# Kernel tuning notes

Measured on AMD Instinct MI355X. Metric: run time of the kernel, lower is better.

## Reference

```python
import jax, jax.numpy as jnp
import numpy as np

B, L, M, IS = 64, 20, 16, 1024  # batch, headers/example, tokens/header, feature dim
EPS = 1e-12


def setup_inputs() -> dict:
    key = jax.random.key(0)
    ks = jax.random.split(key, 10)
    total = B * L
    s = 1.0 / np.sqrt(IS)
    return {
        "ctx": jax.random.normal(ks[0], (B, IS), jnp.float32),
        "wemb_hpu": jax.random.normal(ks[1], (total, M, IS), jnp.float32),
        "l_hpu": jnp.full((total,), M, jnp.int32),
        "l_hs": jnp.full((B,), L, jnp.int32),
        "U_w": jax.random.uniform(ks[2], (IS, IS), jnp.float32, -s, s),
        "U_b": jnp.zeros((IS,), jnp.float32),
        "V_w": jax.random.uniform(ks[3], (IS, IS), jnp.float32, -s, s),
        "V_b": jnp.zeros((IS,), jnp.float32),
        "enc_w": jax.random.uniform(ks[4], (IS, 2 * IS), jnp.float32, -s, s),
        "enc_b": jnp.zeros((IS,), jnp.float32),
        "gamma": jnp.ones((IS,), jnp.float32),
        "beta": jnp.zeros((IS,), jnp.float32),
    }


def reference(ctx, wemb_hpu, l_hpu, l_hs, U_w, U_b, V_w, V_b, enc_w, enc_b, gamma, beta):
    total = wemb_hpu.shape[0]
    bS = ctx.shape[0]
    seg = jnp.repeat(jnp.arange(bS), total // bS)  # header-unit -> example id (constant l_hs)
    wenc_u = ctx @ U_w.T + U_b                      # [B, IS]
    wenc_v = wemb_hpu @ V_w.T + V_b                 # [T, M, IS]
    # per-header attention over its M tokens: sum over feature dim, softmax over tokens
    attn = jnp.einsum('ti,tmi->tm', wenc_u[seg], wenc_v)   # [T, M]
    p = jax.nn.softmax(attn, axis=1)
    pooled = jnp.einsum('tm,tmi->ti', p, wemb_hpu)          # [T, IS]
    cat = jnp.concatenate([pooled, ctx[seg]], axis=-1)      # [T, 2*IS]
    h = cat @ enc_w.T + enc_b                               # [T, IS]
    # scatter into padded [B, mL_hs, IS] (constant lengths -> exact reshape)
    wenc_hs = h.reshape(bS, total // bS, -1)
    # TF-style LayerNorm (eps inside sqrt)
    u = wenc_hs.mean(-1, keepdims=True)
    s2 = ((wenc_hs - u) ** 2).mean(-1, keepdims=True)
    x = (wenc_hs - u) / jnp.sqrt(s2 + EPS)
    return gamma * x + beta
```

## Files before the change

kernel.cpp:

```cpp
#include <hip/hip_runtime.h>
#include <math.h>

#define TPB 256

constexpr int ISZ = 1024;
constexpr int NB  = 64;
constexpr int NL  = 20;
constexpr int NM  = 16;
constexpr int NT  = NB * NL;

typedef __attribute__((ext_vector_type(8))) short  bf16x8;
typedef __attribute__((ext_vector_type(4))) float  f32x4;

__device__ __forceinline__ unsigned short f2bf(float x) {
    unsigned int u = __builtin_bit_cast(unsigned int, x);
    unsigned int r = (u + 0x7fff + ((u >> 16) & 1)) >> 16;
    return (unsigned short)r;
}
__device__ __forceinline__ float bf2f(unsigned short h) {
    unsigned int u = ((unsigned int)h) << 16;
    return __builtin_bit_cast(float, u);
}
__device__ __forceinline__ void split4(float4 v, ushort4& h, ushort4& l) {
    h.x = f2bf(v.x); l.x = f2bf(v.x - bf2f(h.x));
    h.y = f2bf(v.y); l.y = f2bf(v.y - bf2f(h.y));
    h.z = f2bf(v.z); l.z = f2bf(v.z - bf2f(h.z));
    h.w = f2bf(v.w); l.w = f2bf(v.w - bf2f(h.w));
}
__device__ __forceinline__ void gld_lds16(const void* g, void* l) {
    __builtin_amdgcn_global_load_lds(
        (const __attribute__((address_space(1))) unsigned int*)g,
        (__attribute__((address_space(3))) unsigned int*)l, 16, 0, 0);
}


__device__ __forceinline__ void stage_hl(const float* __restrict__ src, int ld,
                                         int kbeg, unsigned char* ldsH,
                                         unsigned char* ldsL, int tid)
{
    #pragma unroll
    for (int r = 0; r < 4; ++r) {
        int idx = r * 256 + tid;
        int row = idx >> 4, cg = (idx & 15) << 2;
        float4 v = *(const float4*)&src[(size_t)row * ld + kbeg + cg];
        ushort4 h, l; split4(v, h, l);
        int boff = row * 128 + ((cg << 1) ^ ((row & 7) << 4));
        *(ushort4*)(ldsH + boff) = h;
        *(ushort4*)(ldsL + boff) = l;
    }
}
__device__ __forceinline__ void stage_h(const float* __restrict__ src, int ld,
                                        int kbeg, unsigned char* ldsH, int tid)
{
    #pragma unroll
    for (int r = 0; r < 4; ++r) {
        int idx = r * 256 + tid;
        int row = idx >> 4, cg = (idx & 15) << 2;
        float4 v = *(const float4*)&src[(size_t)row * ld + kbeg + cg];
        ushort4 h = { f2bf(v.x), f2bf(v.y), f2bf(v.z), f2bf(v.w) };
        int boff = row * 128 + ((cg << 1) ^ ((row & 7) << 4));
        *(ushort4*)(ldsH + boff) = h;
    }
}

__device__ __forceinline__ void comp_hl(const unsigned char* lds, f32x4 acc[2][2], int tid)
{
    const int wid = tid >> 6, lane = tid & 63;
    const int ln = lane & 15, kb = lane >> 4;
    const int wr = wid >> 1, wc = wid & 1;
    #pragma unroll
    for (int ks = 0; ks < 2; ++ks) {
        const int cb = ks * 64 + kb * 16;
        bf16x8 ah[2], al[2], bh[2], bl[2];
        #pragma unroll
        for (int m = 0; m < 2; ++m) {
            int ra = wr * 32 + m * 16 + ln;
            int off = ra * 128 + (cb ^ ((ra & 7) << 4));
            ah[m] = *(const bf16x8*)(lds + off);
            al[m] = *(const bf16x8*)(lds + 8192 + off);
        }
        #pragma unroll
        for (int n = 0; n < 2; ++n) {
            int rb = wc * 32 + n * 16 + ln;
            int off = rb * 128 + (cb ^ ((rb & 7) << 4));
            bh[n] = *(const bf16x8*)(lds + 16384 + off);
            bl[n] = *(const bf16x8*)(lds + 24576 + off);
        }
        #pragma unroll
        for (int m = 0; m < 2; ++m)
            #pragma unroll
            for (int n = 0; n < 2; ++n) {
                acc[m][n] = __builtin_amdgcn_mfma_f32_16x16x32_bf16(ah[m], bh[n], acc[m][n], 0, 0, 0);
                acc[m][n] = __builtin_amdgcn_mfma_f32_16x16x32_bf16(ah[m], bl[n], acc[m][n], 0, 0, 0);
                acc[m][n] = __builtin_amdgcn_mfma_f32_16x16x32_bf16(al[m], bh[n], acc[m][n], 0, 0, 0);
            }
    }
}
__device__ __forceinline__ void comp_h(const unsigned char* lds, f32x4 acc[2][2], int tid)
{
    const int wid = tid >> 6, lane = tid & 63;
    const int ln = lane & 15, kb = lane >> 4;
    const int wr = wid >> 1, wc = wid & 1;
    #pragma unroll
    for (int ks = 0; ks < 2; ++ks) {
        const int cb = ks * 64 + kb * 16;
        bf16x8 ah[2], bh[2];
        #pragma unroll
        for (int m = 0; m < 2; ++m) {
            int ra = wr * 32 + m * 16 + ln;
            ah[m] = *(const bf16x8*)(lds + ra * 128 + (cb ^ ((ra & 7) << 4)));
        }
        #pragma unroll
        for (int n = 0; n < 2; ++n) {
            int rb = wc * 32 + n * 16 + ln;
            bh[n] = *(const bf16x8*)(lds + 16384 + rb * 128 + (cb ^ ((rb & 7) << 4)));
        }
        #pragma unroll
        for (int m = 0; m < 2; ++m)
            #pragma unroll
            for (int n = 0; n < 2; ++n)
                acc[m][n] = __builtin_amdgcn_mfma_f32_16x16x32_bf16(ah[m], bh[n], acc[m][n], 0, 0, 0);
    }
}

__global__ __launch_bounds__(TPB)
void init_small(float* __restrict__ wenc_u, float* __restrict__ cenc,
                float* __restrict__ uv,
                const float* __restrict__ U_b, const float* __restrict__ enc_b)
{
    int i = blockIdx.x * TPB + threadIdx.x;
    int i4 = i << 2;
    int col = i4 & (ISZ - 1);
    if (i4 < NB * ISZ) {
        *(float4*)&wenc_u[i4] = *(const float4*)&U_b[col];
    } else if (i4 < 2 * NB * ISZ) {
        *(float4*)&cenc[i4 - NB * ISZ] = *(const float4*)&enc_b[col];
    } else {
        float4 z = {0.f, 0.f, 0.f, 0.f};
        *(float4*)&uv[i4 - 2 * NB * ISZ] = z;
    }
}

__global__ __launch_bounds__(TPB)
void small_and_vt(const float* __restrict__ ctx, const float* __restrict__ U_w,
                  const float* __restrict__ enc_w, const float* __restrict__ V_w,
                  float* __restrict__ wenc_u, float* __restrict__ cenc,
                  unsigned short* __restrict__ Vth, unsigned short* __restrict__ Vtl)
{
    __shared__ __align__(16) unsigned char smem[32768];
    const int tid = threadIdx.x;
    const int bid = blockIdx.x;

    if (bid >= 256) {
        float (*t)[65] = (float(*)[65])smem;
        const int id = bid - 256;
        const int r0 = (id >> 4) * 64, c0 = (id & 15) * 64;
        const int tr = tid >> 4, tc = (tid & 15) * 4;
        #pragma unroll
        for (int i = 0; i < 4; ++i) {
            float4 v = *(const float4*)&V_w[(size_t)(r0 + tr + 16 * i) * ISZ + c0 + tc];
            t[tr + 16 * i][tc + 0] = v.x; t[tr + 16 * i][tc + 1] = v.y;
            t[tr + 16 * i][tc + 2] = v.z; t[tr + 16 * i][tc + 3] = v.w;
        }
        __syncthreads();
        #pragma unroll
        for (int i = 0; i < 4; ++i) {
            int rr = tr + 16 * i;
            float4 v = { t[tc + 0][rr], t[tc + 1][rr], t[tc + 2][rr], t[tc + 3][rr] };
            ushort4 h, l; split4(v, h, l);
            *(ushort4*)&Vth[(size_t)(c0 + rr) * ISZ + r0 + tc] = h;
            *(ushort4*)&Vtl[(size_t)(c0 + rr) * ISZ + r0 + tc] = l;
        }
        return;
    }

    const int n0 = (bid & 15) * 64;
    const int yv = bid >> 4;
    const bool isU = (yv >= 8);
    const int kbeg = (isU ? (yv - 8) : yv) * 128;

    f32x4 acc[2][2] = {};
    for (int kt = 0; kt < 2; ++kt) {
        const int kk = kbeg + kt * 64;
        if (isU) {
            stage_hl(ctx, ISZ, kk, smem, smem + 8192, tid);
            stage_hl(U_w + (size_t)n0 * ISZ, ISZ, kk, smem + 16384, smem + 24576, tid);
        } else {
            stage_h(ctx, ISZ, kk, smem, tid);
            stage_h(enc_w + (size_t)n0 * 2048 + 1024, 2048, kk, smem + 16384, tid);
        }
        __syncthreads();
        if (isU) comp_hl(smem, acc, tid);
        else     comp_h(smem, acc, tid);
        __syncthreads();
    }

    const int wid = tid >> 6, lane = tid & 63;
    const int wr = wid >> 1, wc = wid & 1;
    const int cl = lane & 15, rg = lane >> 4;
    float* dst = isU ? wenc_u : cenc;
    #pragma unroll
    for (int m = 0; m < 2; ++m)
        #pragma unroll
        for (int n = 0; n < 2; ++n) {
            int col = n0 + wc * 32 + n * 16 + cl;
            #pragma unroll
            for (int j = 0; j < 4; ++j) {
                int row = wr * 32 + m * 16 + rg * 4 + j;
                atomicAdd(&dst[(size_t)row * ISZ + col], acc[m][n][j]);
            }
        }
}

__global__ __launch_bounds__(TPB)
void gemm_uv(const float* __restrict__ wenc_u,
             const unsigned short* __restrict__ Vth,
             const unsigned short* __restrict__ Vtl,
             float* __restrict__ uv)
{
    __shared__ __align__(16) unsigned char smem[32768];
    const int tid = threadIdx.x;
    const int n0 = blockIdx.x * 64;
    const int kbeg = blockIdx.y * 128;
    const int wid = tid >> 6, lane = tid & 63;
    const int srow = lane >> 3, sbyte = (lane & 7) << 4;
    const int swz = sbyte ^ (srow << 4);

    f32x4 acc[2][2] = {};
    for (int kt = 0; kt < 2; ++kt) {
        const int kk = kbeg + kt * 64;
        const int kbyte = kk * 2;
        #pragma unroll
        for (int i = 0; i < 2; ++i) {
            int r = wid * 8 + i * 32 + srow;
            size_t gb = (size_t)(n0 + r) * 2048 + kbyte + swz;
            gld_lds16((const char*)Vth + gb, (void*)(smem + 16384 + wid * 1024 + i * 4096));
            gld_lds16((const char*)Vtl + gb, (void*)(smem + 24576 + wid * 1024 + i * 4096));
        }
        stage_hl(wenc_u, ISZ, kk, smem, smem + 8192, tid);
        __syncthreads();
        comp_hl(smem, acc, tid);
        __syncthreads();
    }

    const int wr = wid >> 1, wc = wid & 1;
    const int cl = lane & 15, rg = lane >> 4;
    #pragma unroll
    for (int m = 0; m < 2; ++m)
        #pragma unroll
        for (int n = 0; n < 2; ++n) {
            int col = n0 + wc * 32 + n * 16 + cl;
            #pragma unroll
            for (int j = 0; j < 4; ++j) {
                int row = wr * 32 + m * 16 + rg * 4 + j;
                atomicAdd(&uv[(size_t)row * ISZ + col], acc[m][n][j]);
            }
        }
}

__global__ __launch_bounds__(TPB)
void attn_encconv(const float* __restrict__ wemb, const float* __restrict__ uv,
                  unsigned short* __restrict__ pooledb,
                  const float* __restrict__ enc_w, unsigned short* __restrict__ encb)
{
    if (blockIdx.x >= NT) {
        const int row = blockIdx.x - NT;
        const int c = threadIdx.x << 2;
        float4 v = *(const float4*)&enc_w[(size_t)row * 2048 + c];
        ushort4 o = { f2bf(v.x), f2bf(v.y), f2bf(v.z), f2bf(v.w) };
        *(ushort4*)&encb[(size_t)row * ISZ + c] = o;
        return;
    }
    const int t   = blockIdx.x;
    const int b   = t / NL;
    const int tid = threadIdx.x;
    const int lane = tid & 63, wid = tid >> 6;
    __shared__ float red[16][4];
    __shared__ float att[16];

    const float* w = wemb + (size_t)t * NM * ISZ;
    const int j0 = tid << 2;
    float4 u4 = *(const float4*)&uv[(size_t)b * ISZ + j0];

    float4 wv[NM];
    float part[NM];
    #pragma unroll
    for (int m = 0; m < NM; ++m) {
        wv[m] = *(const float4*)&w[m * ISZ + j0];
        part[m] = wv[m].x * u4.x + wv[m].y * u4.y + wv[m].z * u4.z + wv[m].w * u4.w;
    }
    #pragma unroll
    for (int m = 0; m < NM; ++m) {
        float v = part[m];
        #pragma unroll
        for (int off = 32; off > 0; off >>= 1) v += __shfl_down(v, off, 64);
        if (lane == 0) red[m][wid] = v;
    }
    __syncthreads();
    if (tid < NM) att[tid] = red[tid][0] + red[tid][1] + red[tid][2] + red[tid][3];
    __syncthreads();

    float mx = att[0];
    #pragma unroll
    for (int m = 1; m < NM; ++m) mx = fmaxf(mx, att[m]);
    float p[NM], s = 0.0f;
    #pragma unroll
    for (int m = 0; m < NM; ++m) { p[m] = __expf(att[m] - mx); s += p[m]; }
    float inv = 1.0f / s;

    float4 acc = {0.0f, 0.0f, 0.0f, 0.0f};
    #pragma unroll
    for (int m = 0; m < NM; ++m) {
        float pm = p[m] * inv;
        acc.x += pm * wv[m].x; acc.y += pm * wv[m].y;
        acc.z += pm * wv[m].z; acc.w += pm * wv[m].w;
    }
    ushort4 o;
    o.x = f2bf(acc.x); o.y = f2bf(acc.y); o.z = f2bf(acc.z); o.w = f2bf(acc.w);
    *(ushort4*)&pooledb[(size_t)t * ISZ + j0] = o;
}

__global__ __launch_bounds__(TPB)
void gemm_enc_mfma(const unsigned short* __restrict__ Abf,
                   const unsigned short* __restrict__ Bbf,
                   const float* __restrict__ cenc,
                   float* __restrict__ C)
{
    __shared__ __align__(16) unsigned char lds[24576];
    const int tid  = threadIdx.x;
    const int wid  = tid >> 6, lane = tid & 63;
    const int m0   = blockIdx.y * 128;
    const int n0   = blockIdx.x * 64;
    const int ln   = lane & 15, kb = lane >> 4;
    const int wr   = wid >> 1, wc = wid & 1;
    const int srow = lane >> 3, sbyte = (lane & 7) << 4;
    const int swz  = sbyte ^ (srow << 4);

    f32x4 acc[4][2] = {};
    const char* Abase = (const char*)Abf;
    const char* Bbase = (const char*)Bbf;

    for (int kt = 0; kt < 16; ++kt) {
        const int kbyte = kt * 128;
        #pragma unroll
        for (int i = 0; i < 4; ++i) {
            int r = wid * 8 + i * 32 + srow;
            gld_lds16(Abase + ((size_t)(m0 + r) * ISZ) * 2 + kbyte + swz,
                      (void*)(lds + wid * 1024 + i * 4096));
        }
        #pragma unroll
        for (int i = 0; i < 2; ++i) {
            int r = wid * 8 + i * 32 + srow;
            gld_lds16(Bbase + ((size_t)(n0 + r) * ISZ) * 2 + kbyte + swz,
                      (void*)(lds + 16384 + wid * 1024 + i * 4096));
        }
        __syncthreads();

        #pragma unroll
        for (int ks = 0; ks < 2; ++ks) {
            const int cb = (ks * 64 + kb * 16);
            bf16x8 a[4], b[2];
            #pragma unroll
            for (int m = 0; m < 4; ++m) {
                int ra = wr * 64 + m * 16 + ln;
                a[m] = *(const bf16x8*)(lds + ra * 128 + (cb ^ ((ra & 7) << 4)));
            }
            #pragma unroll
            for (int n = 0; n < 2; ++n) {
                int rb = wc * 32 + n * 16 + ln;
                b[n] = *(const bf16x8*)(lds + 16384 + rb * 128 + (cb ^ ((rb & 7) << 4)));
            }
            #pragma unroll
            for (int m = 0; m < 4; ++m)
                #pragma unroll
                for (int n = 0; n < 2; ++n)
                    acc[m][n] = __builtin_amdgcn_mfma_f32_16x16x32_bf16(a[m], b[n], acc[m][n], 0, 0, 0);
        }
        __syncthreads();
    }

    const int cl = lane & 15, rg = lane >> 4;
    #pragma unroll
    for (int m = 0; m < 4; ++m) {
        #pragma unroll
        for (int n = 0; n < 2; ++n) {
            int col = n0 + wc * 32 + n * 16 + cl;
            #pragma unroll
            for (int j = 0; j < 4; ++j) {
                int row = m0 + wr * 64 + m * 16 + rg * 4 + j;
                C[(size_t)row * ISZ + col] = acc[m][n][j] + cenc[(size_t)(row / NL) * ISZ + col];
            }
        }
    }
}

__global__ __launch_bounds__(TPB)
void layernorm_inplace(float* __restrict__ x, const float* __restrict__ gamma,
                       const float* __restrict__ beta)
{
    __shared__ float rs[4], rs2[4];
    __shared__ float mu_s, rstd_s;
    const int t = blockIdx.x;
    const int tid = threadIdx.x;
    const int lane = tid & 63, wid = tid >> 6;
    const int c = tid << 2;

    float4 v = *(const float4*)&x[(size_t)t * ISZ + c];
    float s  = v.x + v.y + v.z + v.w;
    float s2 = v.x * v.x + v.y * v.y + v.z * v.z + v.w * v.w;
    #pragma unroll
    for (int off = 32; off > 0; off >>= 1) {
        s  += __shfl_down(s, off, 64);
        s2 += __shfl_down(s2, off, 64);
    }
    if (lane == 0) { rs[wid] = s; rs2[wid] = s2; }
    __syncthreads();
    if (tid == 0) {
        float S  = rs[0] + rs[1] + rs[2] + rs[3];
        float S2 = rs2[0] + rs2[1] + rs2[2] + rs2[3];
        float m  = S / ISZ;
        float var = S2 / ISZ - m * m;
        mu_s  = m;
        rstd_s = rsqrtf(var + 1e-12f);
    }
    __syncthreads();
    const float mu = mu_s, rstd = rstd_s;
    float4 g  = *(const float4*)&gamma[c];
    float4 be = *(const float4*)&beta[c];
    float4 o;
    o.x = g.x * (v.x - mu) * rstd + be.x;
    o.y = g.y * (v.y - mu) * rstd + be.y;
    o.z = g.z * (v.z - mu) * rstd + be.z;
    o.w = g.w * (v.w - mu) * rstd + be.w;
    *(float4*)&x[(size_t)t * ISZ + c] = o;
}

extern "C" void kernel_launch(void* const* d_in, const int* in_sizes, int n_in,
                              void* d_out, int out_size, void* d_ws, size_t ws_size,
                              hipStream_t stream)
{
    const float* ctx   = (const float*)d_in[0];
    const float* wemb  = (const float*)d_in[1];
    const float* U_w   = (const float*)d_in[4];
    const float* U_b   = (const float*)d_in[5];
    const float* V_w   = (const float*)d_in[6];
    const float* enc_w = (const float*)d_in[8];
    const float* enc_b = (const float*)d_in[9];
    const float* gamma = (const float*)d_in[10];
    const float* beta  = (const float*)d_in[11];
    float* out = (float*)d_out;

    float* ws     = (float*)d_ws;
    float* wenc_u = ws;
    float* cenc   = ws + 1 * NB * ISZ;
    float* uv     = ws + 2 * NB * ISZ;
    unsigned short* p = (unsigned short*)(ws + 3 * NB * ISZ);
    unsigned short* Vth     = p;  p += ISZ * ISZ;
    unsigned short* Vtl     = p;  p += ISZ * ISZ;
    unsigned short* encb    = p;  p += ISZ * ISZ;
    unsigned short* pooledb = p;

    init_small<<<(3 * NB * ISZ / 4 + TPB - 1) / TPB, TPB, 0, stream>>>(
        wenc_u, cenc, uv, U_b, enc_b);

    small_and_vt<<<512, TPB, 0, stream>>>(ctx, U_w, enc_w, V_w,
                                          wenc_u, cenc, Vth, Vtl);

    gemm_uv<<<dim3(16, 8), TPB, 0, stream>>>(wenc_u, Vth, Vtl, uv);

    attn_encconv<<<NT + ISZ, TPB, 0, stream>>>(wemb, uv, pooledb, enc_w, encb);

    gemm_enc_mfma<<<dim3(16, 10), TPB, 0, stream>>>(pooledb, encb, cenc, out);

    layernorm_inplace<<<NT, TPB, 0, stream>>>(out, gamma, beta);
}
```

Baseline: 59.77 us.

## Fuse all stages into one cooperative persistent kernel with grid-wide syncs

```diff
diff --git a/kernel.cpp b/kernel.cpp
--- a/kernel.cpp
+++ b/kernel.cpp
@@ -1,7 +1,12 @@
 #include <hip/hip_runtime.h>
+#include <hip/hip_cooperative_groups.h>
 #include <math.h>
 
-#define TPB 256
+namespace cg = cooperative_groups;
+
+#define TPB   256
+#define CGRID 768
+#define NCU   256
 
 constexpr int ISZ = 1024;
 constexpr int NB  = 64;
@@ -12,6 +17,12 @@
 typedef __attribute__((ext_vector_type(8))) short  bf16x8;
 typedef __attribute__((ext_vector_type(4))) float  f32x4;
 
+struct Args {
+    const float *ctx, *wemb, *U_w, *U_b, *V_w, *enc_w, *enc_b, *gamma, *beta;
+    float *Upart, *uv, *cenc, *out;
+    unsigned short *Vth, *Vtl, *encb, *pooledb;
+};
+
 __device__ __forceinline__ unsigned short f2bf(float x) {
     unsigned int u = __builtin_bit_cast(unsigned int, x);
     unsigned int r = (u + 0x7fff + ((u >> 16) & 1)) >> 16;
@@ -33,7 +44,6 @@
         (__attribute__((address_space(3))) unsigned int*)l, 16, 0, 0);
 }
 
-
 __device__ __forceinline__ void stage_hl(const float* __restrict__ src, int ld,
                                          int kbeg, unsigned char* ldsH,
                                          unsigned char* ldsL, int tid)
@@ -41,10 +51,10 @@
     #pragma unroll
     for (int r = 0; r < 4; ++r) {
         int idx = r * 256 + tid;
-        int row = idx >> 4, cg = (idx & 15) << 2;
-        float4 v = *(const float4*)&src[(size_t)row * ld + kbeg + cg];
+        int row = idx >> 4, cg4 = (idx & 15) << 2;
+        float4 v = *(const float4*)&src[(size_t)row * ld + kbeg + cg4];
         ushort4 h, l; split4(v, h, l);
-        int boff = row * 128 + ((cg << 1) ^ ((row & 7) << 4));
+        int boff = row * 128 + ((cg4 << 1) ^ ((row & 7) << 4));
         *(ushort4*)(ldsH + boff) = h;
         *(ushort4*)(ldsL + boff) = l;
     }
@@ -55,11 +65,33 @@
     #pragma unroll
     for (int r = 0; r < 4; ++r) {
         int idx = r * 256 + tid;
-        int row = idx >> 4, cg = (idx & 15) << 2;
-        float4 v = *(const float4*)&src[(size_t)row * ld + kbeg + cg];
+        int row = idx >> 4, cg4 = (idx & 15) << 2;
+        float4 v = *(const float4*)&src[(size_t)row * ld + kbeg + cg4];
         ushort4 h = { f2bf(v.x), f2bf(v.y), f2bf(v.z), f2bf(v.w) };
-        int boff = row * 128 + ((cg << 1) ^ ((row & 7) << 4));
+        int boff = row * 128 + ((cg4 << 1) ^ ((row & 7) << 4));
         *(ushort4*)(ldsH + boff) = h;
+    }
+}
+__device__ __forceinline__ void stage_A_uv(const float* __restrict__ Upart,
+                                           const float* __restrict__ U_b,
+                                           int kbeg, unsigned char* ldsH,
+                                           unsigned char* ldsL, int tid)
+{
+    #pragma unroll
+    for (int r = 0; r < 4; ++r) {
+        int idx = r * 256 + tid;
+        int row = idx >> 4, cg4 = (idx & 15) << 2;
+        int k = kbeg + cg4;
+        float4 v = *(const float4*)&U_b[k];
+        #pragma unroll
+        for (int s = 0; s < 8; ++s) {
+            float4 u = *(const float4*)&Upart[(size_t)(s * 64 + row) * ISZ + k];
+            v.x += u.x; v.y += u.y; v.z += u.z; v.w += u.w;
+        }
+        ushort4 h, l; split4(v, h, l);
+        int boff = row * 128 + ((cg4 << 1) ^ ((row & 7) << 4));
+        *(ushort4*)(ldsH + boff) = h;
+        *(ushort4*)(ldsL + boff) = l;
     }
 }
 
@@ -123,42 +155,52 @@
     }
 }
 
-__global__ __launch_bounds__(TPB)
-void init_small(float* __restrict__ wenc_u, float* __restrict__ cenc,
-                float* __restrict__ uv,
-                const float* __restrict__ U_b, const float* __restrict__ enc_b)
-{
-    int i = blockIdx.x * TPB + threadIdx.x;
-    int i4 = i << 2;
-    int col = i4 & (ISZ - 1);
-    if (i4 < NB * ISZ) {
-        *(float4*)&wenc_u[i4] = *(const float4*)&U_b[col];
-    } else if (i4 < 2 * NB * ISZ) {
-        *(float4*)&cenc[i4 - NB * ISZ] = *(const float4*)&enc_b[col];
-    } else {
-        float4 z = {0.f, 0.f, 0.f, 0.f};
-        *(float4*)&uv[i4 - 2 * NB * ISZ] = z;
-    }
-}
-
-__global__ __launch_bounds__(TPB)
-void small_and_vt(const float* __restrict__ ctx, const float* __restrict__ U_w,
-                  const float* __restrict__ enc_w, const float* __restrict__ V_w,
-                  float* __restrict__ wenc_u, float* __restrict__ cenc,
-                  unsigned short* __restrict__ Vth, unsigned short* __restrict__ Vtl)
-{
-    __shared__ __align__(16) unsigned char smem[32768];
-    const int tid = threadIdx.x;
-    const int bid = blockIdx.x;
-
-    if (bid >= 256) {
+__device__ void p1_task(const Args& A, int task, int tid, unsigned char* smem)
+{
+    const int wid = tid >> 6, lane = tid & 63;
+    const int wr = wid >> 1, wc = wid & 1;
+    const int cl = lane & 15, rg = lane >> 4;
+
+    if (task < 128) {
+        int i4 = (task * TPB + tid) << 2;
+        if (i4 < NB * ISZ) {
+            float4 z = {0.f, 0.f, 0.f, 0.f};
+            *(float4*)&A.uv[i4] = z;
+        } else {
+            *(float4*)&A.cenc[i4 - NB * ISZ] = *(const float4*)&A.enc_b[i4 & (ISZ - 1)];
+        }
+    } else if (task < 256) {
+        const int id = task - 128;
+        const int s = id >> 4, n0 = (id & 15) * 64;
+        const int kbeg = s * 128;
+        f32x4 acc[2][2] = {};
+        for (int kt = 0; kt < 2; ++kt) {
+            const int kk = kbeg + kt * 64;
+            stage_hl(A.ctx, ISZ, kk, smem, smem + 8192, tid);
+            stage_hl(A.U_w + (size_t)n0 * ISZ, ISZ, kk, smem + 16384, smem + 24576, tid);
+            __syncthreads();
+            comp_hl(smem, acc, tid);
+            __syncthreads();
+        }
+        #pragma unroll
+        for (int m = 0; m < 2; ++m)
+            #pragma unroll
+            for (int n = 0; n < 2; ++n) {
+                int col = n0 + wc * 32 + n * 16 + cl;
+                #pragma unroll
+                for (int j = 0; j < 4; ++j) {
+                    int row = wr * 32 + m * 16 + rg * 4 + j;
+                    A.Upart[(size_t)(s * 64 + row) * ISZ + col] = acc[m][n][j];
+                }
+            }
+    } else if (task < 512) {
         float (*t)[65] = (float(*)[65])smem;
-        const int id = bid - 256;
+        const int id = task - 256;
         const int r0 = (id >> 4) * 64, c0 = (id & 15) * 64;
         const int tr = tid >> 4, tc = (tid & 15) * 4;
         #pragma unroll
         for (int i = 0; i < 4; ++i) {
-            float4 v = *(const float4*)&V_w[(size_t)(r0 + tr + 16 * i) * ISZ + c0 + tc];
+            float4 v = *(const float4*)&A.V_w[(size_t)(r0 + tr + 16 * i) * ISZ + c0 + tc];
             t[tr + 16 * i][tc + 0] = v.x; t[tr + 16 * i][tc + 1] = v.y;
             t[tr + 16 * i][tc + 2] = v.z; t[tr + 16 * i][tc + 3] = v.w;
         }
@@ -168,119 +210,98 @@
             int rr = tr + 16 * i;
             float4 v = { t[tc + 0][rr], t[tc + 1][rr], t[tc + 2][rr], t[tc + 3][rr] };
             ushort4 h, l; split4(v, h, l);
-            *(ushort4*)&Vth[(size_t)(c0 + rr) * ISZ + r0 + tc] = h;
-            *(ushort4*)&Vtl[(size_t)(c0 + rr) * ISZ + r0 + tc] = l;
-        }
-        return;
-    }
-
-    const int n0 = (bid & 15) * 64;
-    const int yv = bid >> 4;
-    const bool isU = (yv >= 8);
-    const int kbeg = (isU ? (yv - 8) : yv) * 128;
-
-    f32x4 acc[2][2] = {};
-    for (int kt = 0; kt < 2; ++kt) {
-        const int kk = kbeg + kt * 64;
-        if (isU) {
-            stage_hl(ctx, ISZ, kk, smem, smem + 8192, tid);
-            stage_hl(U_w + (size_t)n0 * ISZ, ISZ, kk, smem + 16384, smem + 24576, tid);
-        } else {
-            stage_h(ctx, ISZ, kk, smem, tid);
-            stage_h(enc_w + (size_t)n0 * 2048 + 1024, 2048, kk, smem + 16384, tid);
+            *(ushort4*)&A.Vth[(size_t)(c0 + rr) * ISZ + r0 + tc] = h;
+            *(ushort4*)&A.Vtl[(size_t)(c0 + rr) * ISZ + r0 + tc] = l;
         }
         __syncthreads();
-        if (isU) comp_hl(smem, acc, tid);
-        else     comp_h(smem, acc, tid);
-        __syncthreads();
-    }
-
+    } else {
+        const int id = task - 512;
+        const int c = tid << 2;
+        #pragma unroll
+        for (int r = 0; r < 4; ++r) {
+            int row = id * 4 + r;
+            float4 v = *(const float4*)&A.enc_w[(size_t)row * 2048 + c];
+            ushort4 o = { f2bf(v.x), f2bf(v.y), f2bf(v.z), f2bf(v.w) };
+            *(ushort4*)&A.encb[(size_t)row * ISZ + c] = o;
+        }
+    }
+}
+
+__device__ void p2_task(const Args& A, int task, int tid, unsigned char* smem)
+{
     const int wid = tid >> 6, lane = tid & 63;
     const int wr = wid >> 1, wc = wid & 1;
     const int cl = lane & 15, rg = lane >> 4;
-    float* dst = isU ? wenc_u : cenc;
-    #pragma unroll
-    for (int m = 0; m < 2; ++m)
-        #pragma unroll
-        for (int n = 0; n < 2; ++n) {
-            int col = n0 + wc * 32 + n * 16 + cl;
-            #pragma unroll
-            for (int j = 0; j < 4; ++j) {
-                int row = wr * 32 + m * 16 + rg * 4 + j;
-                atomicAdd(&dst[(size_t)row * ISZ + col], acc[m][n][j]);
-            }
-        }
-}
-
-__global__ __launch_bounds__(TPB)
-void gemm_uv(const float* __restrict__ wenc_u,
-             const unsigned short* __restrict__ Vth,
-             const unsigned short* __restrict__ Vtl,
-             float* __restrict__ uv)
-{
-    __shared__ __align__(16) unsigned char smem[32768];
-    const int tid = threadIdx.x;
-    const int n0 = blockIdx.x * 64;
-    const int kbeg = blockIdx.y * 128;
-    const int wid = tid >> 6, lane = tid & 63;
-    const int srow = lane >> 3, sbyte = (lane & 7) << 4;
-    const int swz = sbyte ^ (srow << 4);
-
-    f32x4 acc[2][2] = {};
-    for (int kt = 0; kt < 2; ++kt) {
-        const int kk = kbeg + kt * 64;
-        const int kbyte = kk * 2;
-        #pragma unroll
-        for (int i = 0; i < 2; ++i) {
-            int r = wid * 8 + i * 32 + srow;
-            size_t gb = (size_t)(n0 + r) * 2048 + kbyte + swz;
-            gld_lds16((const char*)Vth + gb, (void*)(smem + 16384 + wid * 1024 + i * 4096));
-            gld_lds16((const char*)Vtl + gb, (void*)(smem + 24576 + wid * 1024 + i * 4096));
-        }
-        stage_hl(wenc_u, ISZ, kk, smem, smem + 8192, tid);
-        __syncthreads();
-        comp_hl(smem, acc, tid);
-        __syncthreads();
-    }
-
-    const int wr = wid >> 1, wc = wid & 1;
-    const int cl = lane & 15, rg = lane >> 4;
-    #pragma unroll
-    for (int m = 0; m < 2; ++m)
-        #pragma unroll
-        for (int n = 0; n < 2; ++n) {
-            int col = n0 + wc * 32 + n * 16 + cl;
-            #pragma unroll
-            for (int j = 0; j < 4; ++j) {
-                int row = wr * 32 + m * 16 + rg * 4 + j;
-                atomicAdd(&uv[(size_t)row * ISZ + col], acc[m][n][j]);
-            }
-        }
-}
-
-__global__ __launch_bounds__(TPB)
-void attn_encconv(const float* __restrict__ wemb, const float* __restrict__ uv,
-                  unsigned short* __restrict__ pooledb,
-                  const float* __restrict__ enc_w, unsigned short* __restrict__ encb)
-{
-    if (blockIdx.x >= NT) {
-        const int row = blockIdx.x - NT;
-        const int c = threadIdx.x << 2;
-        float4 v = *(const float4*)&enc_w[(size_t)row * 2048 + c];
-        ushort4 o = { f2bf(v.x), f2bf(v.y), f2bf(v.z), f2bf(v.w) };
-        *(ushort4*)&encb[(size_t)row * ISZ + c] = o;
-        return;
-    }
-    const int t   = blockIdx.x;
-    const int b   = t / NL;
-    const int tid = threadIdx.x;
+
+    if (task < 128) {
+        const int s = task >> 4, n0 = (task & 15) * 64;
+        const int kbeg = s * 128;
+        const int srow = lane >> 3, sbyte = (lane & 7) << 4;
+        const int swz = sbyte ^ (srow << 4);
+        f32x4 acc[2][2] = {};
+        for (int kt = 0; kt < 2; ++kt) {
+            const int kk = kbeg + kt * 64;
+            const int kbyte = kk * 2;
+            #pragma unroll
+            for (int i = 0; i < 2; ++i) {
+                int r = wid * 8 + i * 32 + srow;
+                size_t gb = (size_t)(n0 + r) * 2048 + kbyte + swz;
+                gld_lds16((const char*)A.Vth + gb, (void*)(smem + 16384 + wid * 1024 + i * 4096));
+                gld_lds16((const char*)A.Vtl + gb, (void*)(smem + 24576 + wid * 1024 + i * 4096));
+            }
+            stage_A_uv(A.Upart, A.U_b, kk, smem, smem + 8192, tid);
+            __syncthreads();
+            comp_hl(smem, acc, tid);
+            __syncthreads();
+        }
+        #pragma unroll
+        for (int m = 0; m < 2; ++m)
+            #pragma unroll
+            for (int n = 0; n < 2; ++n) {
+                int col = n0 + wc * 32 + n * 16 + cl;
+                #pragma unroll
+                for (int j = 0; j < 4; ++j) {
+                    int row = wr * 32 + m * 16 + rg * 4 + j;
+                    atomicAdd(&A.uv[(size_t)row * ISZ + col], acc[m][n][j]);
+                }
+            }
+    } else {
+        const int id = task - 128;
+        const int s = id >> 4, n0 = (id & 15) * 64;
+        const int kbeg = s * 128;
+        f32x4 acc[2][2] = {};
+        for (int kt = 0; kt < 2; ++kt) {
+            const int kk = kbeg + kt * 64;
+            stage_h(A.ctx, ISZ, kk, smem, tid);
+            stage_h(A.enc_w + (size_t)n0 * 2048 + 1024, 2048, kk, smem + 16384, tid);
+            __syncthreads();
+            comp_h(smem, acc, tid);
+            __syncthreads();
+        }
+        #pragma unroll
+        for (int m = 0; m < 2; ++m)
+            #pragma unroll
+            for (int n = 0; n < 2; ++n) {
+                int col = n0 + wc * 32 + n * 16 + cl;
+                #pragma unroll
+                for (int j = 0; j < 4; ++j) {
+                    int row = wr * 32 + m * 16 + rg * 4 + j;
+                    atomicAdd(&A.cenc[(size_t)row * ISZ + col], acc[m][n][j]);
+                }
+            }
+    }
+}
+
+__device__ void p3_task(const Args& A, int t, int tid, unsigned char* smem)
+{
+    float (*red)[4] = (float(*)[4])smem;
+    float* att = (float*)(smem + 256);
+    const int b = t / NL;
     const int lane = tid & 63, wid = tid >> 6;
-    __shared__ float red[16][4];
-    __shared__ float att[16];
-
-    const float* w = wemb + (size_t)t * NM * ISZ;
+
+    const float* w = A.wemb + (size_t)t * NM * ISZ;
     const int j0 = tid << 2;
-    float4 u4 = *(const float4*)&uv[(size_t)b * ISZ + j0];
+    float4 u4 = *(const float4*)&A.uv[(size_t)b * ISZ + j0];
 
     float4 wv[NM];
     float part[NM];
@@ -303,10 +324,10 @@
     float mx = att[0];
     #pragma unroll
     for (int m = 1; m < NM; ++m) mx = fmaxf(mx, att[m]);
-    float p[NM], s = 0.0f;
-    #pragma unroll
-    for (int m = 0; m < NM; ++m) { p[m] = __expf(att[m] - mx); s += p[m]; }
-    float inv = 1.0f / s;
+    float p[NM], sm = 0.0f;
+    #pragma unroll
+    for (int m = 0; m < NM; ++m) { p[m] = __expf(att[m] - mx); sm += p[m]; }
+    float inv = 1.0f / sm;
 
     float4 acc = {0.0f, 0.0f, 0.0f, 0.0f};
     #pragma unroll
@@ -317,28 +338,24 @@
     }
     ushort4 o;
     o.x = f2bf(acc.x); o.y = f2bf(acc.y); o.z = f2bf(acc.z); o.w = f2bf(acc.w);
-    *(ushort4*)&pooledb[(size_t)t * ISZ + j0] = o;
-}
-
-__global__ __launch_bounds__(TPB)
-void gemm_enc_mfma(const unsigned short* __restrict__ Abf,
-                   const unsigned short* __restrict__ Bbf,
-                   const float* __restrict__ cenc,
-                   float* __restrict__ C)
-{
-    __shared__ __align__(16) unsigned char lds[24576];
-    const int tid  = threadIdx.x;
-    const int wid  = tid >> 6, lane = tid & 63;
-    const int m0   = blockIdx.y * 128;
-    const int n0   = blockIdx.x * 64;
-    const int ln   = lane & 15, kb = lane >> 4;
-    const int wr   = wid >> 1, wc = wid & 1;
+    *(ushort4*)&A.pooledb[(size_t)t * ISZ + j0] = o;
+    __syncthreads();
+}
+
+__device__ void p4_task(const Args& A, int task, int tid, unsigned char* smem)
+{
+    const int wid = tid >> 6, lane = tid & 63;
+    const int wr = wid >> 1, wc = wid & 1;
+    const int cl = lane & 15, rg = lane >> 4;
+    const int m0 = (task >> 4) * 128;
+    const int n0 = (task & 15) * 64;
+    const int ln = lane & 15, kb = lane >> 4;
     const int srow = lane >> 3, sbyte = (lane & 7) << 4;
-    const int swz  = sbyte ^ (srow << 4);
+    const int swz = sbyte ^ (srow << 4);
 
     f32x4 acc[4][2] = {};
-    const char* Abase = (const char*)Abf;
-    const char* Bbase = (const char*)Bbf;
+    const char* Abase = (const char*)A.pooledb;
+    const char* Bbase = (const char*)A.encb;
 
     for (int kt = 0; kt < 16; ++kt) {
         const int kbyte = kt * 128;
@@ -346,16 +363,15 @@
         for (int i = 0; i < 4; ++i) {
             int r = wid * 8 + i * 32 + srow;
             gld_lds16(Abase + ((size_t)(m0 + r) * ISZ) * 2 + kbyte + swz,
-                      (void*)(lds + wid * 1024 + i * 4096));
+                      (void*)(smem + wid * 1024 + i * 4096));
         }
         #pragma unroll
         for (int i = 0; i < 2; ++i) {
             int r = wid * 8 + i * 32 + srow;
             gld_lds16(Bbase + ((size_t)(n0 + r) * ISZ) * 2 + kbyte + swz,
-                      (void*)(lds + 16384 + wid * 1024 + i * 4096));
+                      (void*)(smem + 16384 + wid * 1024 + i * 4096));
         }
         __syncthreads();
-
         #pragma unroll
         for (int ks = 0; ks < 2; ++ks) {
             const int cb = (ks * 64 + kb * 16);
@@ -363,12 +379,12 @@
             #pragma unroll
             for (int m = 0; m < 4; ++m) {
                 int ra = wr * 64 + m * 16 + ln;
-                a[m] = *(const bf16x8*)(lds + ra * 128 + (cb ^ ((ra & 7) << 4)));
+                a[m] = *(const bf16x8*)(smem + ra * 128 + (cb ^ ((ra & 7) << 4)));
             }
             #pragma unroll
             for (int n = 0; n < 2; ++n) {
                 int rb = wc * 32 + n * 16 + ln;
-                b[n] = *(const bf16x8*)(lds + 16384 + rb * 128 + (cb ^ ((rb & 7) << 4)));
+                b[n] = *(const bf16x8*)(smem + 16384 + rb * 128 + (cb ^ ((rb & 7) << 4)));
             }
             #pragma unroll
             for (int m = 0; m < 4; ++m)
@@ -378,8 +394,6 @@
         }
         __syncthreads();
     }
-
-    const int cl = lane & 15, rg = lane >> 4;
     #pragma unroll
     for (int m = 0; m < 4; ++m) {
         #pragma unroll
@@ -388,24 +402,21 @@
             #pragma unroll
             for (int j = 0; j < 4; ++j) {
                 int row = m0 + wr * 64 + m * 16 + rg * 4 + j;
-                C[(size_t)row * ISZ + col] = acc[m][n][j] + cenc[(size_t)(row / NL) * ISZ + col];
-            }
-        }
-    }
-}
-
-__global__ __launch_bounds__(TPB)
-void layernorm_inplace(float* __restrict__ x, const float* __restrict__ gamma,
-                       const float* __restrict__ beta)
-{
-    __shared__ float rs[4], rs2[4];
-    __shared__ float mu_s, rstd_s;
-    const int t = blockIdx.x;
-    const int tid = threadIdx.x;
+                A.out[(size_t)row * ISZ + col] = acc[m][n][j] + A.cenc[(size_t)(row / NL) * ISZ + col];
+            }
+        }
+    }
+}
+
+__device__ void p5_task(const Args& A, int t, int tid, unsigned char* smem)
+{
+    float* rs  = (float*)smem;
+    float* rs2 = (float*)(smem + 16);
+    float* mus = (float*)(smem + 32);
     const int lane = tid & 63, wid = tid >> 6;
     const int c = tid << 2;
 
-    float4 v = *(const float4*)&x[(size_t)t * ISZ + c];
+    float4 v = *(const float4*)&A.out[(size_t)t * ISZ + c];
     float s  = v.x + v.y + v.z + v.w;
     float s2 = v.x * v.x + v.y * v.y + v.z * v.z + v.w * v.w;
     #pragma unroll
@@ -420,57 +431,98 @@
         float S2 = rs2[0] + rs2[1] + rs2[2] + rs2[3];
         float m  = S / ISZ;
         float var = S2 / ISZ - m * m;
-        mu_s  = m;
-        rstd_s = rsqrtf(var + 1e-12f);
+        mus[0] = m;
+        mus[1] = rsqrtf(var + 1e-12f);
     }
     __syncthreads();
-    const float mu = mu_s, rstd = rstd_s;
-    float4 g  = *(const float4*)&gamma[c];
-    float4 be = *(const float4*)&beta[c];
+    const float mu = mus[0], rstd = mus[1];
+    float4 g  = *(const float4*)&A.gamma[c];
+    float4 be = *(const float4*)&A.beta[c];
     float4 o;
     o.x = g.x * (v.x - mu) * rstd + be.x;
     o.y = g.y * (v.y - mu) * rstd + be.y;
     o.z = g.z * (v.z - mu) * rstd + be.z;
     o.w = g.w * (v.w - mu) * rstd + be.w;
-    *(float4*)&x[(size_t)t * ISZ + c] = o;
+    *(float4*)&A.out[(size_t)t * ISZ + c] = o;
+    __syncthreads();
+}
+
+__global__ __launch_bounds__(TPB, 4)
+void fused_all(Args A)
+{
+    cg::grid_group grid = cg::this_grid();
+    __shared__ __align__(16) unsigned char smem[32768];
+    const int tid = threadIdx.x;
+
+    for (int t = blockIdx.x; t < 768; t += gridDim.x) p1_task(A, t, tid, smem);
+    grid.sync();
+    for (int t = blockIdx.x; t < 256; t += gridDim.x) p2_task(A, t, tid, smem);
+    grid.sync();
+    for (int t = blockIdx.x; t < NT;  t += gridDim.x) p3_task(A, t, tid, smem);
+    grid.sync();
+    for (int t = blockIdx.x; t < 160; t += gridDim.x) p4_task(A, t, tid, smem);
+    grid.sync();
+    for (int t = blockIdx.x; t < NT;  t += gridDim.x) p5_task(A, t, tid, smem);
+}
+
+__global__ __launch_bounds__(TPB) void k_p1(Args A) {
+    __shared__ __align__(16) unsigned char smem[32768];
+    p1_task(A, blockIdx.x, threadIdx.x, smem);
+}
+__global__ __launch_bounds__(TPB) void k_p2(Args A) {
+    __shared__ __align__(16) unsigned char smem[32768];
+    p2_task(A, blockIdx.x, threadIdx.x, smem);
+}
+__global__ __launch_bounds__(TPB) void k_p3(Args A) {
+    __shared__ __align__(16) unsigned char smem[512];
+    p3_task(A, blockIdx.x, threadIdx.x, smem);
+}
+__global__ __launch_bounds__(TPB) void k_p4(Args A) {
+    __shared__ __align__(16) unsigned char smem[24576];
+    p4_task(A, blockIdx.x, threadIdx.x, smem);
+}
+__global__ __launch_bounds__(TPB) void k_p5(Args A) {
+    __shared__ __align__(16) unsigned char smem[512];
+    p5_task(A, blockIdx.x, threadIdx.x, smem);
 }
 
 extern "C" void kernel_launch(void* const* d_in, const int* in_sizes, int n_in,
                               void* d_out, int out_size, void* d_ws, size_t ws_size,
                               hipStream_t stream)
 {
-    const float* ctx   = (const float*)d_in[0];
-    const float* wemb  = (const float*)d_in[1];
-    const float* U_w   = (const float*)d_in[4];
-    const float* U_b   = (const float*)d_in[5];
-    const float* V_w   = (const float*)d_in[6];
-    const float* enc_w = (const float*)d_in[8];
-    const float* enc_b = (const float*)d_in[9];
-    const float* gamma = (const float*)d_in[10];
-    const float* beta  = (const float*)d_in[11];
-    float* out = (float*)d_out;
-
-    float* ws     = (float*)d_ws;
-    float* wenc_u = ws;
-    float* cenc   = ws + 1 * NB * ISZ;
-    float* uv     = ws + 2 * NB * ISZ;
-    unsigned short* p = (unsigned short*)(ws + 3 * NB * ISZ);
-    unsigned short* Vth     = p;  p += ISZ * ISZ;
-    unsigned short* Vtl     = p;  p += ISZ * ISZ;
-    unsigned short* encb    = p;  p += ISZ * ISZ;
-    unsigned short* pooledb = p;
-
-    init_small<<<(3 * NB * ISZ / 4 + TPB - 1) / TPB, TPB, 0, stream>>>(
-        wenc_u, cenc, uv, U_b, enc_b);
-
-    small_and_vt<<<512, TPB, 0, stream>>>(ctx, U_w, enc_w, V_w,
-                                          wenc_u, cenc, Vth, Vtl);
-
-    gemm_uv<<<dim3(16, 8), TPB, 0, stream>>>(wenc_u, Vth, Vtl, uv);
-
-    attn_encconv<<<NT + ISZ, TPB, 0, stream>>>(wemb, uv, pooledb, enc_w, encb);
-
-    gemm_enc_mfma<<<dim3(16, 10), TPB, 0, stream>>>(pooledb, encb, cenc, out);
-
-    layernorm_inplace<<<NT, TPB, 0, stream>>>(out, gamma, beta);
-}
+    Args A;
+    A.ctx   = (const float*)d_in[0];
+    A.wemb  = (const float*)d_in[1];
+    A.U_w   = (const float*)d_in[4];
+    A.U_b   = (const float*)d_in[5];
+    A.V_w   = (const float*)d_in[6];
+    A.enc_w = (const float*)d_in[8];
+    A.enc_b = (const float*)d_in[9];
+    A.gamma = (const float*)d_in[10];
+    A.beta  = (const float*)d_in[11];
+    A.out   = (float*)d_out;
+
+    float* ws = (float*)d_ws;
+    A.Upart = ws;
+    A.uv    = ws + 8 * NB * ISZ;
+    A.cenc  = A.uv + NB * ISZ;
+    unsigned short* p = (unsigned short*)(A.cenc + NB * ISZ);
+    A.Vth     = p;  p += ISZ * ISZ;
+    A.Vtl     = p;  p += ISZ * ISZ;
+    A.encb    = p;  p += ISZ * ISZ;
+    A.pooledb = p;
+
+    int nb = 0;
+    hipError_t qe = hipOccupancyMaxActiveBlocksPerMultiprocessor(&nb, fused_all, TPB, 0);
+    if (qe == hipSuccess && nb * NCU >= CGRID) {
+        void* kargs[] = { (void*)&A };
+        hipLaunchCooperativeKernel((const void*)fused_all, dim3(CGRID), dim3(TPB),
+                                   kargs, 0, stream);
+    } else {
+        k_p1<<<768, TPB, 0, stream>>>(A);
+        k_p2<<<256, TPB, 0, stream>>>(A);
+        k_p3<<<NT,  TPB, 0, stream>>>(A);
+        k_p4<<<160, TPB, 0, stream>>>(A);
+        k_p5<<<NT,  TPB, 0, stream>>>(A);
+    }
+}
```

Result: slower. 64.34 us (+7.6%).
